# Performance work log

Hardware: AMD Instinct MI355X
Metric: run time of the kernel (lower is better)

Reference implementation:

```python
import jax, jax.numpy as jnp
import numpy as np

NUM_JOINTS = 140
NUM_VERTICES = 13059
NUM_BONES = 28
BATCH = 512


def euler_zyx_to_rot(e):
    """e: [..., 3] Euler angles in (z, y, x) order -> [..., 3, 3] with R = Rz @ Ry @ Rx."""
    z, y, x = e[..., 0], e[..., 1], e[..., 2]
    cx, sx = jnp.cos(x), jnp.sin(x)
    cy, sy = jnp.cos(y), jnp.sin(y)
    cz, sz = jnp.cos(z), jnp.sin(z)
    r00 = cz * cy
    r01 = cz * sy * sx - sz * cx
    r02 = cz * sy * cx + sz * sx
    r10 = sz * cy
    r11 = sz * sy * sx + cz * cx
    r12 = sz * sy * cx - cz * sx
    r20 = -sy
    r21 = cy * sx
    r22 = cy * cx
    R = jnp.stack([r00, r01, r02, r10, r11, r12, r20, r21, r22], axis=-1)
    return R.reshape(e.shape[:-1] + (3, 3))


def _mouse_forward(pose, bone_lengths, center_bone_length, trans, scale,
                   v_template, t_pose_joints, weights, parent, bone_mapper):
    B = pose.shape[0]
    Jn = NUM_JOINTS
    dt = pose.dtype

    bl = jax.nn.sigmoid(bone_lengths / 5.0) * 2.0            # [B, 28]
    R = euler_zyx_to_rot(pose.reshape(B, Jn, 3))             # [B, J, 3, 3]
    Jt = t_pose_joints                                       # [J, 3]

    # bone offsets for joints 1..J-1, scaled per bone_length_mapper
    off = Jt[1:] - Jt[parent[1:]]                            # [J-1, 3]
    blid = bone_mapper[1:]                                   # [J-1]
    bl_g = jnp.where(blid[None, :] >= 0,
                     jnp.take(bl, jnp.maximum(blid, 0), axis=1),
                     jnp.ones((), dt))                       # [B, J-1]
    # joint index 1 (position 0 in the [J-1] arrays) uses center_bone_length
    scale_per = bl_g.at[:, 0].set(center_bone_length[:, 0])
    off_b = off[None] * scale_per[..., None]                 # [B, J-1, 3]

    bottom = jnp.broadcast_to(jnp.array([0., 0., 0., 1.], dt), (B, Jn - 1, 1, 4))
    top = jnp.concatenate([R[:, 1:], off_b[..., None]], axis=-1)   # [B, J-1, 3, 4]
    A = jnp.concatenate([top, bottom], axis=-2)              # [B, J-1, 4, 4] local transforms

    root_t = jnp.broadcast_to(Jt[0], (B, 3))[..., None]      # [B, 3, 1]
    root_top = jnp.concatenate([R[:, 0], root_t], axis=-1)   # [B, 3, 4]
    root_bot = jnp.broadcast_to(jnp.array([0., 0., 0., 1.], dt), (B, 1, 4))
    G0 = jnp.concatenate([root_top, root_bot], axis=-2)      # [B, 4, 4]

    G_init = jnp.zeros((B, Jn, 4, 4), dt).at[:, 0].set(G0)

    def step(G, xs):
        i, p, Ai = xs                                        # Ai: [B, 4, 4]
        Gp = jnp.take(G, p, axis=1)                          # [B, 4, 4]
        Gi = Gp @ Ai
        return G.at[:, i].set(Gi), None

    idx = jnp.arange(1, Jn)
    G, _ = jax.lax.scan(step, G_init, (idx, parent[1:], jnp.swapaxes(A, 0, 1)))

    J_final = G[:, :, :3, 3]                                 # [B, J, 3]

    # subtract rest-pose joint contribution (relative transforms for LBS)
    Jh = jnp.concatenate([jnp.broadcast_to(Jt, (B, Jn, 3)),
                          jnp.zeros((B, Jn, 1), dt)], axis=-1)      # [B, J, 4]
    d = jnp.einsum('bjmn,bjn->bjm', G, Jh)                   # [B, J, 4]
    G_rel = jnp.concatenate([G[..., :3], (G[..., 3] - d)[..., None]], axis=-1)

    # linear blend skinning
    T = jnp.einsum('vj,bjmn->bvmn', weights, G_rel)          # [B, V, 4, 4]
    vh = jnp.concatenate([v_template, jnp.ones((NUM_VERTICES, 1), dt)], axis=-1)
    V = jnp.einsum('bvmn,vn->bvm', T[:, :, :3, :], vh)       # [B, V, 3]

    s = scale[:, 0][:, None, None]
    V = V * s + trans[:, None, :]
    J_out = J_final * s + trans[:, None, :]
    return V, J_out


def setup_inputs() -> dict:
    key = jax.random.key(0)
    ks = jax.random.split(key, 8)
    rng = np.random.default_rng(0)
    parent = np.zeros(NUM_JOINTS, dtype=np.int32)
    for i in range(1, NUM_JOINTS):
        parent[i] = rng.integers(0, i)                       # valid kinematic tree
    bone_mapper = rng.integers(-1, NUM_BONES, size=NUM_JOINTS).astype(np.int32)
    W = jax.random.uniform(ks[6], (NUM_VERTICES, NUM_JOINTS), jnp.float32)
    W = W / jnp.sum(W, axis=1, keepdims=True)                # row-stochastic skinning weights
    return {
        'pose': jax.random.normal(ks[0], (BATCH, NUM_JOINTS * 3), jnp.float32) * 0.2,
        'bone_lengths': jax.random.normal(ks[1], (BATCH, NUM_BONES), jnp.float32),
        'center_bone_length': jax.random.uniform(ks[2], (BATCH, 1), jnp.float32, 0.5, 1.5),
        'trans': jax.random.normal(ks[3], (BATCH, 3), jnp.float32),
        'scale': jax.random.uniform(ks[4], (BATCH, 1), jnp.float32, 0.5, 1.5),
        'v_template': jax.random.normal(ks[5], (NUM_VERTICES, 3), jnp.float32),
        't_pose_joints': jax.random.normal(ks[7], (NUM_JOINTS, 3), jnp.float32),
        'weights': W,
        'parent': jnp.asarray(parent),
        'bone_mapper': jnp.asarray(bone_mapper),
    }


def reference(pose, bone_lengths, center_bone_length, trans, scale,
              v_template, t_pose_joints, weights, parent, bone_mapper):
    return _mouse_forward(pose, bone_lengths, center_bone_length, trans, scale,
                          v_template, t_pose_joints, weights, parent, bone_mapper)
```

## Files before the change

kernel.cpp:

```cpp
#include <hip/hip_runtime.h>
#include <math.h>

#define NJ 140
#define NV 13059
#define NB 512
#define NBONES 28

#define MTILES 103
#define NBLK 12
#define KS 18
#define GRID_GEMM (MTILES*NBLK)

#define APREP_SLOTS (MTILES*KS*512)
#define PREPB (APREP_SLOTS/256)

typedef _Float16 f16x8 __attribute__((ext_vector_type(8)));
typedef float    f32x4 __attribute__((ext_vector_type(4)));

#define GL16(gp, lp) __builtin_amdgcn_global_load_lds( \
    (const __attribute__((address_space(1))) unsigned int*)(gp), \
    (__attribute__((address_space(3))) unsigned int*)(lp), 16, 0, 0)

__global__ __launch_bounds__(256) void prep_kin_kernel(
    const float* __restrict__ pose,
    const float* __restrict__ bone_lengths,
    const float* __restrict__ cbl,
    const float* __restrict__ trans,
    const float* __restrict__ scale,
    const float* __restrict__ v_template,
    const float* __restrict__ t_pose,
    const int*   __restrict__ parent,
    const int*   __restrict__ bone_mapper,
    const float* __restrict__ weights,
    _Float16* __restrict__ Ap,
    _Float16* __restrict__ Bp,
    float* __restrict__ jout)
{
    const int t = threadIdx.x;

    if (blockIdx.x >= 512) {
        int tg   = (blockIdx.x - 512) * 256 + t;
        int mt   = tg / (KS*512);
        int r    = tg - mt*(KS*512);
        int ks   = r >> 9;
        int slot = r & 511;
        int row  = slot >> 2;
        int cs   = slot & 3;
        int ci   = cs ^ ((row >> 1) & 3);
        int v    = mt*128 + row;
        int j0   = ks*8 + ci*2;
        f16x8 out;
        #pragma unroll
        for (int i = 0; i < 8; ++i) out[i] = (_Float16)0.f;
        if (v < NV) {
            float x = v_template[v*3+0];
            float y = v_template[v*3+1];
            float z = v_template[v*3+2];
            if (j0 < NJ) {
                float w0 = weights[(size_t)v*NJ + j0];
                out[0] = (_Float16)(w0*x); out[1] = (_Float16)(w0*y);
                out[2] = (_Float16)(w0*z); out[3] = (_Float16)w0;
            }
            if (j0 + 1 < NJ) {
                float w1 = weights[(size_t)v*NJ + j0 + 1];
                out[4] = (_Float16)(w1*x); out[5] = (_Float16)(w1*y);
                out[6] = (_Float16)(w1*z); out[7] = (_Float16)w1;
            }
        }
        *(f16x8*)(Ap + (size_t)tg * 8) = out;
        return;
    }

    __shared__ float M0[NJ][12];
    __shared__ float M1[NJ][12];
    __shared__ int   a0[NJ];
    __shared__ int   a1[NJ];

    const int b = blockIdx.x;

    if (t < NJ) {
        const int j = t;
        float z = pose[b*(NJ*3) + 3*j + 0];
        float y = pose[b*(NJ*3) + 3*j + 1];
        float x = pose[b*(NJ*3) + 3*j + 2];
        float cx = cosf(x), sx = sinf(x);
        float cy = cosf(y), sy = sinf(y);
        float cz = cosf(z), sz = sinf(z);
        float r00 = cz*cy;
        float r01 = cz*sy*sx - sz*cx;
        float r02 = cz*sy*cx + sz*sx;
        float r10 = sz*cy;
        float r11 = sz*sy*sx + cz*cx;
        float r12 = sz*sy*cx - cz*sx;
        float r20 = -sy;
        float r21 = cy*sx;
        float r22 = cy*cx;
        float t0, t1, t2;
        int p = parent[j];
        if (j == 0) {
            t0 = t_pose[0]; t1 = t_pose[1]; t2 = t_pose[2];
        } else {
            float ox = t_pose[3*j+0] - t_pose[3*p+0];
            float oy = t_pose[3*j+1] - t_pose[3*p+1];
            float oz = t_pose[3*j+2] - t_pose[3*p+2];
            float s;
            if (j == 1) {
                s = cbl[b];
            } else {
                int blid = bone_mapper[j];
                if (blid >= 0) {
                    float bv = bone_lengths[b*NBONES + blid];
                    s = 2.0f / (1.0f + expf(-bv*0.2f));
                } else {
                    s = 1.0f;
                }
            }
            t0 = ox*s; t1 = oy*s; t2 = oz*s;
        }
        M0[j][0]=r00; M0[j][1]=r01; M0[j][2]=r02;  M0[j][3]=t0;
        M0[j][4]=r10; M0[j][5]=r11; M0[j][6]=r12;  M0[j][7]=t1;
        M0[j][8]=r20; M0[j][9]=r21; M0[j][10]=r22; M0[j][11]=t2;
        a0[j] = (j == 0) ? -1 : p;
    }
    __syncthreads();

    float* src = &M0[0][0]; float* dst = &M1[0][0];
    int* as = a0; int* ad = a1;
    for (int r = 0; r < 8; ++r) {
        if (t < NJ) {
            int a = as[t];
            const float* Mi = src + t*12;
            float* Do = dst + t*12;
            if (a >= 0) {
                const float* Mp = src + a*12;
                #pragma unroll
                for (int m = 0; m < 3; ++m) {
                    float p0 = Mp[m*4+0], p1 = Mp[m*4+1], p2 = Mp[m*4+2], p3 = Mp[m*4+3];
                    Do[m*4+0] = p0*Mi[0] + p1*Mi[4] + p2*Mi[8];
                    Do[m*4+1] = p0*Mi[1] + p1*Mi[5] + p2*Mi[9];
                    Do[m*4+2] = p0*Mi[2] + p1*Mi[6] + p2*Mi[10];
                    Do[m*4+3] = p0*Mi[3] + p1*Mi[7] + p2*Mi[11] + p3;
                }
                ad[t] = as[a];
            } else {
                #pragma unroll
                for (int e = 0; e < 12; ++e) Do[e] = Mi[e];
                ad[t] = -1;
            }
        }
        __syncthreads();
        float* tf = src; src = dst; dst = tf;
        int* ti = as; as = ad; ad = ti;
    }

    float* grl = dst;
    if (t < NJ) {
        const int j = t;
        const float* G = src + j*12;
        float sb = scale[b];
        float tr0 = trans[b*3+0], tr1 = trans[b*3+1], tr2 = trans[b*3+2];
        float* jo = jout + ((size_t)b*NJ + j)*3;
        jo[0] = G[3]*sb  + tr0;
        jo[1] = G[7]*sb  + tr1;
        jo[2] = G[11]*sb + tr2;
        float jx = t_pose[3*j+0], jy = t_pose[3*j+1], jz = t_pose[3*j+2];
        #pragma unroll
        for (int c = 0; c < 3; ++c) {
            float g0 = G[c*4+0], g1 = G[c*4+1], g2 = G[c*4+2];
            float g3 = G[c*4+3] - (g0*jx + g1*jy + g2*jz);
            grl[j*12 + c*4 + 0] = g0;
            grl[j*12 + c*4 + 1] = g1;
            grl[j*12 + c*4 + 2] = g2;
            grl[j*12 + c*4 + 3] = g3;
        }
    }
    __syncthreads();

    if (t < 216) {
        int c  = t / 72;
        int rr = t - c*72;
        int ks = rr >> 2;
        int ci = rr & 3;
        int nrow = b*3 + c;
        int nb = nrow >> 7;
        int rl = nrow & 127;
        int j0 = ks*8 + ci*2;
        f16x8 o;
        #pragma unroll
        for (int i = 0; i < 8; ++i) o[i] = (_Float16)0.f;
        if (j0 < NJ) {
            o[0] = (_Float16)grl[j0*12 + c*4 + 0];
            o[1] = (_Float16)grl[j0*12 + c*4 + 1];
            o[2] = (_Float16)grl[j0*12 + c*4 + 2];
            o[3] = (_Float16)grl[j0*12 + c*4 + 3];
        }
        if (j0 + 1 < NJ) {
            o[4] = (_Float16)grl[(j0+1)*12 + c*4 + 0];
            o[5] = (_Float16)grl[(j0+1)*12 + c*4 + 1];
            o[6] = (_Float16)grl[(j0+1)*12 + c*4 + 2];
            o[7] = (_Float16)grl[(j0+1)*12 + c*4 + 3];
        }
        int cs = ci ^ ((rl >> 1) & 3);
        *(f16x8*)(Bp + ((size_t)(nb*KS + ks)*512 + rl*4 + cs)*8) = o;
    }
}

__global__ __launch_bounds__(256) void gemm_kernel(
    const _Float16* __restrict__ Ap,
    const _Float16* __restrict__ Bp,
    const float* __restrict__ scale,
    const float* __restrict__ trans,
    float* __restrict__ vout)
{
    __shared__ _Float16 sA[2][4096];
    __shared__ _Float16 sB[2][4096];

    const int t    = threadIdx.x;
    const int lane = t & 63;
    const int wid  = t >> 6;
    const int ln   = lane & 15;
    const int kq   = lane >> 4;
    const int wm   = wid & 1;
    const int wn   = wid >> 1;

    const int mt = blockIdx.x / NBLK;
    const int nb = blockIdx.x % NBLK;

    const _Float16* Ag = Ap + (size_t)mt*(KS*4096);
    const _Float16* Bg = Bp + (size_t)nb*(KS*4096);

    const int c1 = wid*64 + lane;
    const int c2 = c1 + 256;
    const int lb1 = wid*512;
    const int lb2 = 2048 + wid*512;

    const int csl = kq ^ ((ln >> 1) & 3);
    const int rA  = wm*64 + ln;
    const int rB  = wn*64 + ln;
    const int afo = rA*32 + csl*8;
    const int bfo = rB*32 + csl*8;

    f32x4 acc[4][4];
    #pragma unroll
    for (int mi = 0; mi < 4; ++mi)
        #pragma unroll
        for (int ni = 0; ni < 4; ++ni)
            acc[mi][ni] = (f32x4){0.f, 0.f, 0.f, 0.f};

    long long obase[4]; float es[4], etr[4];
    #pragma unroll
    for (int ni = 0; ni < 4; ++ni) {
        int n  = nb*128 + wn*64 + ni*16 + ln;
        int bq = n / 3;
        int cr = n - bq*3;
        obase[ni] = (long long)bq*(NV*3) + cr;
        es[ni]  = scale[bq];
        etr[ni] = trans[n];
    }

    auto stage = [&](int buf, int ks) {
        const _Float16* a = Ag + ks*4096;
        const _Float16* b = Bg + ks*4096;
        GL16(a + c1*8, &sA[buf][lb1]);
        GL16(a + c2*8, &sA[buf][lb2]);
        GL16(b + c1*8, &sB[buf][lb1]);
        GL16(b + c2*8, &sB[buf][lb2]);
    };
    auto compute = [&](int buf) {
        f16x8 af[4], bf[4];
        #pragma unroll
        for (int mi = 0; mi < 4; ++mi)
            af[mi] = *(const f16x8*)&sA[buf][afo + mi*512];
        #pragma unroll
        for (int ni = 0; ni < 4; ++ni)
            bf[ni] = *(const f16x8*)&sB[buf][bfo + ni*512];
        #pragma unroll
        for (int mi = 0; mi < 4; ++mi)
            #pragma unroll
            for (int ni = 0; ni < 4; ++ni)
                acc[mi][ni] = __builtin_amdgcn_mfma_f32_16x16x32_f16(
                    af[mi], bf[ni], acc[mi][ni], 0, 0, 0);
    };

    stage(0, 0);
    #pragma unroll 1
    for (int ks = 0; ks < KS; ks += 2) {
        __syncthreads();
        if (ks + 1 < KS) stage(1, ks + 1);
        compute(0);
        __syncthreads();
        if (ks + 2 < KS) stage(0, ks + 2);
        compute(1);
    }

    const int vb = mt*128 + wm*64 + kq*4;
    #pragma unroll
    for (int mi = 0; mi < 4; ++mi) {
        #pragma unroll
        for (int ni = 0; ni < 4; ++ni) {
            #pragma unroll
            for (int r = 0; r < 4; ++r) {
                int vg = vb + mi*16 + r;
                if (vg < NV)
                    vout[obase[ni] + (long long)vg*3] =
                        acc[mi][ni][r]*es[ni] + etr[ni];
            }
        }
    }
}

extern "C" void kernel_launch(void* const* d_in, const int* in_sizes, int n_in,
                              void* d_out, int out_size, void* d_ws, size_t ws_size,
                              hipStream_t stream) {
    const float* pose         = (const float*)d_in[0];
    const float* bone_lengths = (const float*)d_in[1];
    const float* cbl          = (const float*)d_in[2];
    const float* trans        = (const float*)d_in[3];
    const float* scale        = (const float*)d_in[4];
    const float* v_template   = (const float*)d_in[5];
    const float* t_pose       = (const float*)d_in[6];
    const float* weights      = (const float*)d_in[7];
    const int*   parent       = (const int*)d_in[8];
    const int*   bone_mapper  = (const int*)d_in[9];

    float* vout = (float*)d_out;
    float* jout = vout + (size_t)NB*NV*3;

    _Float16* Ap = (_Float16*)d_ws;
    _Float16* Bp = Ap + (size_t)APREP_SLOTS*8;

    prep_kin_kernel<<<512 + PREPB, 256, 0, stream>>>(
        pose, bone_lengths, cbl, trans, scale, v_template, t_pose,
        parent, bone_mapper, weights, Ap, Bp, jout);

    gemm_kernel<<<GRID_GEMM, 256, 0, stream>>>(Ap, Bp, scale, trans, vout);
}
```

Before: 167.0 us.

## Triple-buffer GEMM with vmcnt waits, XCD block remap, separate vectorized A-prep

The GEMM main loop moves from a double-buffered `__syncthreads` pipeline to a three-stage LDS ring. Each step waits on `s_waitcnt vmcnt(4)` plus a raw barrier, so two tiles of global-to-LDS loads stay in flight during compute. Block indices are remapped so consecutive tiles land on the same XCD for better L2 reuse, and the scale/trans epilogue loads move after the main loop to ease register pressure. The weight×vertex A-operand prep becomes its own kernel that reads weights as float4 and writes two swizzled chunks per thread. The cost is one extra kernel launch and more LDS per GEMM block.

```diff
diff --git a/kernel.cpp b/kernel.cpp
--- a/kernel.cpp
+++ b/kernel.cpp
@@ -12,7 +12,6 @@
 #define GRID_GEMM (MTILES*NBLK)
 
 #define APREP_SLOTS (MTILES*KS*512)
-#define PREPB (APREP_SLOTS/256)
 
 typedef _Float16 f16x8 __attribute__((ext_vector_type(8)));
 typedef float    f32x4 __attribute__((ext_vector_type(4)));
@@ -21,55 +20,19 @@
     (const __attribute__((address_space(1))) unsigned int*)(gp), \
     (__attribute__((address_space(3))) unsigned int*)(lp), 16, 0, 0)
 
-__global__ __launch_bounds__(256) void prep_kin_kernel(
+__global__ __launch_bounds__(256) void kin_kernel(
     const float* __restrict__ pose,
     const float* __restrict__ bone_lengths,
     const float* __restrict__ cbl,
     const float* __restrict__ trans,
     const float* __restrict__ scale,
-    const float* __restrict__ v_template,
     const float* __restrict__ t_pose,
     const int*   __restrict__ parent,
     const int*   __restrict__ bone_mapper,
-    const float* __restrict__ weights,
-    _Float16* __restrict__ Ap,
     _Float16* __restrict__ Bp,
     float* __restrict__ jout)
 {
     const int t = threadIdx.x;
-
-    if (blockIdx.x >= 512) {
-        int tg   = (blockIdx.x - 512) * 256 + t;
-        int mt   = tg / (KS*512);
-        int r    = tg - mt*(KS*512);
-        int ks   = r >> 9;
-        int slot = r & 511;
-        int row  = slot >> 2;
-        int cs   = slot & 3;
-        int ci   = cs ^ ((row >> 1) & 3);
-        int v    = mt*128 + row;
-        int j0   = ks*8 + ci*2;
-        f16x8 out;
-        #pragma unroll
-        for (int i = 0; i < 8; ++i) out[i] = (_Float16)0.f;
-        if (v < NV) {
-            float x = v_template[v*3+0];
-            float y = v_template[v*3+1];
-            float z = v_template[v*3+2];
-            if (j0 < NJ) {
-                float w0 = weights[(size_t)v*NJ + j0];
-                out[0] = (_Float16)(w0*x); out[1] = (_Float16)(w0*y);
-                out[2] = (_Float16)(w0*z); out[3] = (_Float16)w0;
-            }
-            if (j0 + 1 < NJ) {
-                float w1 = weights[(size_t)v*NJ + j0 + 1];
-                out[4] = (_Float16)(w1*x); out[5] = (_Float16)(w1*y);
-                out[6] = (_Float16)(w1*z); out[7] = (_Float16)w1;
-            }
-        }
-        *(f16x8*)(Ap + (size_t)tg * 8) = out;
-        return;
-    }
 
     __shared__ float M0[NJ][12];
     __shared__ float M1[NJ][12];
@@ -205,6 +168,50 @@
     }
 }
 
+__global__ __launch_bounds__(256) void aprep_kernel(
+    const float* __restrict__ v_template,
+    const float* __restrict__ weights,
+    _Float16* __restrict__ Ap)
+{
+    const int t   = threadIdx.x;
+    const int mt  = blockIdx.x / KS;
+    const int ks  = blockIdx.x - mt*KS;
+    const int row = t >> 1;
+    const int q   = t & 1;
+    const int v   = mt*128 + row;
+    const int j0  = ks*8 + q*4;
+    const int s   = (row >> 1) & 3;
+
+    f16x8 oA, oB;
+    #pragma unroll
+    for (int i = 0; i < 8; ++i) { oA[i] = (_Float16)0.f; oB[i] = (_Float16)0.f; }
+
+    if (v < NV && j0 + 3 < NJ) {
+        float x = v_template[v*3+0];
+        float y = v_template[v*3+1];
+        float z = v_template[v*3+2];
+        const float4 w4 = *(const float4*)(weights + (size_t)v*NJ + j0);
+        oA[0] = (_Float16)(w4.x*x); oA[1] = (_Float16)(w4.x*y);
+        oA[2] = (_Float16)(w4.x*z); oA[3] = (_Float16)w4.x;
+        oA[4] = (_Float16)(w4.y*x); oA[5] = (_Float16)(w4.y*y);
+        oA[6] = (_Float16)(w4.y*z); oA[7] = (_Float16)w4.y;
+        oB[0] = (_Float16)(w4.z*x); oB[1] = (_Float16)(w4.z*y);
+        oB[2] = (_Float16)(w4.z*z); oB[3] = (_Float16)w4.z;
+        oB[4] = (_Float16)(w4.w*x); oB[5] = (_Float16)(w4.w*y);
+        oB[6] = (_Float16)(w4.w*z); oB[7] = (_Float16)w4.w;
+    }
+
+    const int base = ((2*q) ^ s) & ~1;
+    _Float16* dst = Ap + (((size_t)blockIdx.x)*512 + row*4 + base)*8;
+    if (s & 1) {
+        *(f16x8*)dst       = oB;
+        *(f16x8*)(dst + 8) = oA;
+    } else {
+        *(f16x8*)dst       = oA;
+        *(f16x8*)(dst + 8) = oB;
+    }
+}
+
 __global__ __launch_bounds__(256) void gemm_kernel(
     const _Float16* __restrict__ Ap,
     const _Float16* __restrict__ Bp,
@@ -212,8 +219,8 @@
     const float* __restrict__ trans,
     float* __restrict__ vout)
 {
-    __shared__ _Float16 sA[2][4096];
-    __shared__ _Float16 sB[2][4096];
+    __shared__ _Float16 sA[3][4096];
+    __shared__ _Float16 sB[3][4096];
 
     const int t    = threadIdx.x;
     const int lane = t & 63;
@@ -223,8 +230,14 @@
     const int wm   = wid & 1;
     const int wn   = wid >> 1;
 
-    const int mt = blockIdx.x / NBLK;
-    const int nb = blockIdx.x % NBLK;
+    const int q8 = GRID_GEMM >> 3;
+    const int r8 = GRID_GEMM & 7;
+    const int xcd = blockIdx.x & 7;
+    const int idx = blockIdx.x >> 3;
+    const int wgid = (xcd < r8 ? xcd*(q8+1) : r8*(q8+1) + (xcd-r8)*q8) + idx;
+
+    const int mt = wgid / NBLK;
+    const int nb = wgid - mt*NBLK;
 
     const _Float16* Ag = Ap + (size_t)mt*(KS*4096);
     const _Float16* Bg = Bp + (size_t)nb*(KS*4096);
@@ -246,17 +259,6 @@
         #pragma unroll
         for (int ni = 0; ni < 4; ++ni)
             acc[mi][ni] = (f32x4){0.f, 0.f, 0.f, 0.f};
-
-    long long obase[4]; float es[4], etr[4];
-    #pragma unroll
-    for (int ni = 0; ni < 4; ++ni) {
-        int n  = nb*128 + wn*64 + ni*16 + ln;
-        int bq = n / 3;
-        int cr = n - bq*3;
-        obase[ni] = (long long)bq*(NV*3) + cr;
-        es[ni]  = scale[bq];
-        etr[ni] = trans[n];
-    }
 
     auto stage = [&](int buf, int ks) {
         const _Float16* a = Ag + ks*4096;
@@ -282,17 +284,35 @@
                     af[mi], bf[ni], acc[mi][ni], 0, 0, 0);
     };
 
+    #define WAITBAR4 do { \
+        asm volatile("s_waitcnt vmcnt(4)" ::: "memory"); \
+        __builtin_amdgcn_s_barrier(); } while (0)
+
     stage(0, 0);
+    stage(1, 1);
     #pragma unroll 1
-    for (int ks = 0; ks < KS; ks += 2) {
-        __syncthreads();
-        if (ks + 1 < KS) stage(1, ks + 1);
-        compute(0);
-        __syncthreads();
-        if (ks + 2 < KS) stage(0, ks + 2);
-        compute(1);
-    }
-
+    for (int ks = 0; ks < KS - 3; ks += 3) {
+        WAITBAR4; stage(2, ks + 2); compute(0);
+        WAITBAR4; stage(0, ks + 3); compute(1);
+        WAITBAR4; stage(1, ks + 4); compute(2);
+    }
+    WAITBAR4; stage(2, 17); compute(0);
+    WAITBAR4; compute(1);
+    asm volatile("s_waitcnt vmcnt(0)" ::: "memory");
+    __builtin_amdgcn_s_barrier();
+    compute(2);
+    #undef WAITBAR4
+
+    long long obase[4]; float es[4], etr[4];
+    #pragma unroll
+    for (int ni = 0; ni < 4; ++ni) {
+        int n  = nb*128 + wn*64 + ni*16 + ln;
+        int bq = n / 3;
+        int cr = n - bq*3;
+        obase[ni] = (long long)bq*(NV*3) + cr;
+        es[ni]  = scale[bq];
+        etr[ni] = trans[n];
+    }
     const int vb = mt*128 + wm*64 + kq*4;
     #pragma unroll
     for (int mi = 0; mi < 4; ++mi) {
@@ -329,9 +349,9 @@
     _Float16* Ap = (_Float16*)d_ws;
     _Float16* Bp = Ap + (size_t)APREP_SLOTS*8;
 
-    prep_kin_kernel<<<512 + PREPB, 256, 0, stream>>>(
-        pose, bone_lengths, cbl, trans, scale, v_template, t_pose,
-        parent, bone_mapper, weights, Ap, Bp, jout);
-
+    aprep_kernel<<<MTILES*KS, 256, 0, stream>>>(v_template, weights, Ap);
+    kin_kernel<<<NB, 256, 0, stream>>>(
+        pose, bone_lengths, cbl, trans, scale, t_pose,
+        parent, bone_mapper, Bp, jout);
     gemm_kernel<<<GRID_GEMM, 256, 0, stream>>>(Ap, Bp, scale, trans, vout);
 }
```

Measured after the change: 179.0 us. +7.2%, slower.
